# Kernel optimization log

Measured on AMD Instinct MI355X. Metric: run time of the kernel, lower is better.

Reference implementation:

```python
import jax, jax.numpy as jnp
import numpy as np

B, N, C, K, D, H = 4, 16384, 256, 16, 4, 512
EPS = 1e-5


def setup_inputs() -> dict:
    key = jax.random.key(0)
    ks = jax.random.split(key, 16)
    s = 0.05  # weight scale
    inp = {
        "x": jax.random.normal(ks[0], (B, N, C), jnp.float32),
        "knn": jax.random.randint(ks[1], (B, N, K), 0, N, jnp.int32),
        "lfp_w": jax.random.normal(ks[2], (D, C, C), jnp.float32) * s,
        "lfp_bn_w": jax.random.uniform(ks[3], (D, C), jnp.float32),
        "lfp_bn_b": jax.random.normal(ks[4], (D, C), jnp.float32) * s,
        "mlp0_w1": jax.random.normal(ks[5], (C, H), jnp.float32) * s,
        "mlp0_b1": jax.random.normal(ks[6], (H,), jnp.float32) * s,
        "mlp0_w2": jax.random.normal(ks[7], (H, C), jnp.float32) * s,
        "mlp0_bn_w": jax.random.uniform(ks[8], (C,), jnp.float32),
        "mlp0_bn_b": jax.random.normal(ks[9], (C,), jnp.float32) * s,
        "mlps_w1": jax.random.normal(ks[10], (D // 2, C, H), jnp.float32) * s,
        "mlps_b1": jax.random.normal(ks[11], (D // 2, H), jnp.float32) * s,
        "mlps_w2": jax.random.normal(ks[12], (D // 2, H, C), jnp.float32) * s,
        "mlps_bn_w": jax.random.uniform(ks[13], (D // 2, C), jnp.float32),
        "mlps_bn_b": jax.random.normal(ks[14], (D // 2, C), jnp.float32) * s,
    }
    return inp


def _bn(y, w, b):
    # BatchNorm1d over flattened (B*N) rows, biased variance, train-mode stats
    m = y.mean(axis=(0, 1))
    v = ((y - m) ** 2).mean(axis=(0, 1))
    return (y - m) * jax.lax.rsqrt(v + EPS) * w + b


def _mlp(y, w1, b1, w2, bw, bb):
    h = jax.nn.gelu(jnp.einsum("bnc,ch->bnh", y, w1) + b1, approximate=False)
    return _bn(jnp.einsum("bnh,hc->bnc", h, w2), bw, bb)


def _lfp(y, knn, w, bw, bb):
    p = jnp.einsum("bnc,cd->bnd", y, w)               # linear proj, no bias
    nb = jax.vmap(lambda pb, kb: pb[kb])(p, knn)      # [B,N,K,C] neighbor gather
    return _bn(nb.max(axis=2) - p, bw, bb)            # max over knn minus self


def reference(x, knn, lfp_w, lfp_bn_w, lfp_bn_b,
              mlp0_w1, mlp0_b1, mlp0_w2, mlp0_bn_w, mlp0_bn_b,
              mlps_w1, mlps_b1, mlps_w2, mlps_bn_w, mlps_bn_b):
    # Block.forward (eval: drop_path = identity)
    x = x + _mlp(x, mlp0_w1, mlp0_b1, mlp0_w2, mlp0_bn_w, mlp0_bn_b)
    depth = lfp_w.shape[0]
    for i in range(depth):
        x = x + _lfp(x, knn, lfp_w[i], lfp_bn_w[i], lfp_bn_b[i])
        if i % 2 == 1:
            j = i // 2
            x = x + _mlp(x, mlps_w1[j], mlps_b1[j], mlps_w2[j],
                         mlps_bn_w[j], mlps_bn_b[j])
    return x
```

## Files before the change

### kernel.cpp

```cpp
#include <hip/hip_runtime.h>
#include <hip/hip_bf16.h>

#define M_TOTAL 65536
#define NPTS    16384
#define CDIM    256
#define KNN     16
#define HDIM    512

typedef __bf16 bf16x8 __attribute__((ext_vector_type(8)));
typedef float  f32x4  __attribute__((ext_vector_type(4)));

__device__ inline float b2f(unsigned u) {
    union { unsigned v; float f; } x; x.v = u << 16; return x.f;
}
__device__ inline unsigned short f2b(float f) {
    union { float f; unsigned u; } x; x.f = f;
    unsigned r = x.u + 0x7fffu + ((x.u >> 16) & 1u);
    return (unsigned short)(r >> 16);
}
__device__ inline void gload_lds16(const void* g, void* l) {
    __builtin_amdgcn_global_load_lds(
        (const __attribute__((address_space(1))) unsigned*)g,
        (__attribute__((address_space(3))) unsigned*)l, 16, 0, 0);
}

template<int MODE>
__global__ __launch_bounds__(256) void gemm_nt(
    const short* __restrict__ A, const short* __restrict__ BT,
    short* __restrict__ outB,
    const float* __restrict__ bias, float2* __restrict__ partials,
    int N, int K)
{
    __shared__ short a_lds[128 * 32];
    __shared__ short b_lds[128 * 32];
    __shared__ float s_sum[128], s_sq[128];

    const int tid = threadIdx.x;
    const int m0 = blockIdx.y * 128, n0 = blockIdx.x * 128;
    const int w = tid >> 6, l = tid & 63;
    const int wm = w >> 1, wn = w & 1;

    if (MODE == 2 && tid < 128) { s_sum[tid] = 0.f; s_sq[tid] = 0.f; }

    f32x4 acc[4][4] = {};

    const int lrow = l & 15, lk = (l >> 4) * 8;
    const int q0 = 2 * w, q1 = 2 * w + 1;
    const int gr = l >> 2, gc = (l & 3) * 8;
    const size_t arow0 = (size_t)(m0 + q0 * 16 + gr) * K + gc;
    const size_t arow1 = (size_t)(m0 + q1 * 16 + gr) * K + gc;
    const size_t brow0 = (size_t)(n0 + q0 * 16 + gr) * K + gc;
    const size_t brow1 = (size_t)(n0 + q1 * 16 + gr) * K + gc;

    const int nkt = K >> 5;
    for (int kt = 0; kt < nkt; ++kt) {
        const int k0 = kt << 5;
        if (kt) __syncthreads();
        gload_lds16(A  + arow0 + k0, a_lds + q0 * 512);
        gload_lds16(A  + arow1 + k0, a_lds + q1 * 512);
        gload_lds16(BT + brow0 + k0, b_lds + q0 * 512);
        gload_lds16(BT + brow1 + k0, b_lds + q1 * 512);
        __syncthreads();

        bf16x8 af[4], bfr[4];
#pragma unroll
        for (int i = 0; i < 4; ++i)
            af[i] = *(const bf16x8*)(a_lds + (wm * 64 + i * 16 + lrow) * 32 + lk);
#pragma unroll
        for (int j = 0; j < 4; ++j)
            bfr[j] = *(const bf16x8*)(b_lds + (wn * 64 + j * 16 + lrow) * 32 + lk);
#pragma unroll
        for (int i = 0; i < 4; ++i)
#pragma unroll
            for (int j = 0; j < 4; ++j)
                acc[i][j] = __builtin_amdgcn_mfma_f32_16x16x32_bf16(
                    af[i], bfr[j], acc[i][j], 0, 0, 0);
    }

    const int lq = l >> 4;
#pragma unroll
    for (int j = 0; j < 4; ++j) {
        const int cl  = wn * 64 + j * 16 + lrow;
        const int col = n0 + cl;
        const float bsv = (MODE == 1) ? bias[col] : 0.f;
        float psum = 0.f, psq = 0.f;
#pragma unroll
        for (int i = 0; i < 4; ++i) {
#pragma unroll
            for (int r = 0; r < 4; ++r) {
                const int row = m0 + wm * 64 + i * 16 + lq * 4 + r;
                float v = acc[i][j][r];
                if (MODE == 1) {
                    v += bsv;
                    v = 0.5f * v * (1.f + erff(v * 0.70710678118654752f));
                }
                outB[(size_t)row * N + col] = (short)f2b(v);
                if (MODE == 2) { psum += v; psq += v * v; }
            }
        }
        if (MODE == 2) {
            atomicAdd(&s_sum[cl], psum);
            atomicAdd(&s_sq[cl], psq);
        }
    }
    if (MODE == 2) {
        __syncthreads();
        if (tid < 128)
            partials[(size_t)blockIdx.y * N + n0 + tid] =
                make_float2(s_sum[tid], s_sq[tid]);
    }
}

__global__ __launch_bounds__(256) void gather_max(
    const short* __restrict__ p, const int* __restrict__ knn,
    short* __restrict__ yout, float2* __restrict__ partials)
{
    __shared__ float s_sum[256], s_sq[256];
    const int tid = threadIdx.x, w = tid >> 6, l = tid & 63;
    s_sum[tid] = 0.f; s_sq[tid] = 0.f;
    __syncthreads();

    const int xcd = blockIdx.x & 7, hi = blockIdx.x >> 3;
    const int gblk = (xcd >> 1) * 512 + (hi << 1) + (xcd & 1);

    float sa0 = 0, sa1 = 0, sa2 = 0, sa3 = 0;
    float qa0 = 0, qa1 = 0, qa2 = 0, qa3 = 0;
    const int c0 = l * 4;
    for (int rr = 0; rr < 8; ++rr) {
        const size_t g = (size_t)gblk * 32 + w * 8 + rr;
        const int b = (int)(g >> 14);
        const int n = (int)(g & (NPTS - 1));
        const int4* kp4 = (const int4*)(knn + ((size_t)b * NPTS + n) * KNN);
        int idxs[16];
        {
            const int4 i0 = kp4[0], i1 = kp4[1], i2 = kp4[2], i3 = kp4[3];
            idxs[0]=i0.x; idxs[1]=i0.y; idxs[2]=i0.z; idxs[3]=i0.w;
            idxs[4]=i1.x; idxs[5]=i1.y; idxs[6]=i1.z; idxs[7]=i1.w;
            idxs[8]=i2.x; idxs[9]=i2.y; idxs[10]=i2.z; idxs[11]=i2.w;
            idxs[12]=i3.x; idxs[13]=i3.y; idxs[14]=i3.z; idxs[15]=i3.w;
        }
        const size_t pbase = (size_t)b * NPTS * CDIM;
        float mx0 = -1e30f, mx1 = -1e30f, mx2 = -1e30f, mx3 = -1e30f;
#pragma unroll
        for (int k = 0; k < KNN; ++k) {
            const uint2 v = *(const uint2*)(p + pbase + (size_t)idxs[k] * CDIM + c0);
            mx0 = fmaxf(mx0, b2f(v.x & 0xffffu));
            mx1 = fmaxf(mx1, b2f(v.x >> 16));
            mx2 = fmaxf(mx2, b2f(v.y & 0xffffu));
            mx3 = fmaxf(mx3, b2f(v.y >> 16));
        }
        const uint2 sv = *(const uint2*)(p + g * CDIM + c0);
        const float t0 = mx0 - b2f(sv.x & 0xffffu);
        const float t1 = mx1 - b2f(sv.x >> 16);
        const float t2 = mx2 - b2f(sv.y & 0xffffu);
        const float t3 = mx3 - b2f(sv.y >> 16);
        uint2 pk;
        pk.x = (unsigned)f2b(t0) | ((unsigned)f2b(t1) << 16);
        pk.y = (unsigned)f2b(t2) | ((unsigned)f2b(t3) << 16);
        *(uint2*)(yout + g * CDIM + c0) = pk;
        sa0 += t0; sa1 += t1; sa2 += t2; sa3 += t3;
        qa0 += t0 * t0; qa1 += t1 * t1; qa2 += t2 * t2; qa3 += t3 * t3;
    }
    atomicAdd(&s_sum[c0 + 0], sa0); atomicAdd(&s_sq[c0 + 0], qa0);
    atomicAdd(&s_sum[c0 + 1], sa1); atomicAdd(&s_sq[c0 + 1], qa1);
    atomicAdd(&s_sum[c0 + 2], sa2); atomicAdd(&s_sq[c0 + 2], qa2);
    atomicAdd(&s_sum[c0 + 3], sa3); atomicAdd(&s_sq[c0 + 3], qa3);
    __syncthreads();
    partials[(size_t)gblk * CDIM + tid] = make_float2(s_sum[tid], s_sq[tid]);
}

__global__ __launch_bounds__(256) void reduce_stats(
    const float2* __restrict__ partials, int nblk,
    const float* __restrict__ bnw, const float* __restrict__ bnb,
    float2* __restrict__ scsh)
{
    __shared__ float ss[4], qq[4];
    const int c = blockIdx.x;
    const int tid = threadIdx.x, w = tid >> 6, l = tid & 63;
    float s = 0.f, q = 0.f;
    for (int rb = tid; rb < nblk; rb += 256) {
        const float2 v = partials[(size_t)rb * CDIM + c];
        s += v.x; q += v.y;
    }
#pragma unroll
    for (int off = 32; off > 0; off >>= 1) {
        s += __shfl_down(s, off);
        q += __shfl_down(q, off);
    }
    if (l == 0) { ss[w] = s; qq[w] = q; }
    __syncthreads();
    if (tid == 0) {
        const float S = ss[0] + ss[1] + ss[2] + ss[3];
        const float Q = qq[0] + qq[1] + qq[2] + qq[3];
        const float invM = 1.f / 65536.f;
        const float mean = S * invM;
        const float var  = Q * invM - mean * mean;
        const float istd = rsqrtf(var + 1e-5f);
        const float sc   = bnw[c] * istd;
        scsh[c] = make_float2(sc, bnb[c] - mean * sc);
    }
}

__global__ __launch_bounds__(256) void bn_residual(
    const short* __restrict__ y, const float* __restrict__ resid,
    const float2* __restrict__ scsh,
    float* __restrict__ xout, short* __restrict__ xbout)
{
    const size_t t = (size_t)blockIdx.x * 256 + threadIdx.x;
    const uint2 yv = ((const uint2*)y)[t];
    const float4 rv = ((const float4*)resid)[t];
    const int c0 = (int)((t * 4) & (CDIM - 1));
    const float2 s0 = scsh[c0], s1 = scsh[c0 + 1], s2 = scsh[c0 + 2], s3 = scsh[c0 + 3];
    const float o0 = rv.x + b2f(yv.x & 0xffffu) * s0.x + s0.y;
    const float o1 = rv.y + b2f(yv.x >> 16)     * s1.x + s1.y;
    const float o2 = rv.z + b2f(yv.y & 0xffffu) * s2.x + s2.y;
    const float o3 = rv.w + b2f(yv.y >> 16)     * s3.x + s3.y;
    ((float4*)xout)[t] = make_float4(o0, o1, o2, o3);
    if (xbout) {
        uint2 pk;
        pk.x = (unsigned)f2b(o0) | ((unsigned)f2b(o1) << 16);
        pk.y = (unsigned)f2b(o2) | ((unsigned)f2b(o3) << 16);
        ((uint2*)xbout)[t] = pk;
    }
}

__global__ __launch_bounds__(256) void cast_x(
    const float* __restrict__ x, short* __restrict__ xb)
{
    const size_t t = (size_t)blockIdx.x * 256 + threadIdx.x;
    const float4 v = ((const float4*)x)[t];
    uint2 pk;
    pk.x = (unsigned)f2b(v.x) | ((unsigned)f2b(v.y) << 16);
    pk.y = (unsigned)f2b(v.z) | ((unsigned)f2b(v.w) << 16);
    ((uint2*)xb)[t] = pk;
}

__global__ __launch_bounds__(256) void transpose_cast(
    const float* __restrict__ src, short* __restrict__ dst, int R, int Cc)
{
    const size_t base = (size_t)blockIdx.y * R * Cc;
    const int i = blockIdx.x * 256 + threadIdx.x;
    if (i < R * Cc) {
        const int r = i / Cc, c = i % Cc;
        dst[base + (size_t)c * R + r] = (short)f2b(src[base + i]);
    }
}


extern "C" void kernel_launch(void* const* d_in, const int* in_sizes, int n_in,
                              void* d_out, int out_size, void* d_ws, size_t ws_size,
                              hipStream_t stream)
{
    (void)in_sizes; (void)n_in; (void)out_size; (void)ws_size;

    const float* x_in      = (const float*)d_in[0];
    const int*   knn       = (const int*)  d_in[1];
    const float* lfp_w     = (const float*)d_in[2];
    const float* lfp_bn_w  = (const float*)d_in[3];
    const float* lfp_bn_b  = (const float*)d_in[4];
    const float* mlp0_w1   = (const float*)d_in[5];
    const float* mlp0_b1   = (const float*)d_in[6];
    const float* mlp0_w2   = (const float*)d_in[7];
    const float* mlp0_bn_w = (const float*)d_in[8];
    const float* mlp0_bn_b = (const float*)d_in[9];
    const float* mlps_w1   = (const float*)d_in[10];
    const float* mlps_b1   = (const float*)d_in[11];
    const float* mlps_w2   = (const float*)d_in[12];
    const float* mlps_bn_w = (const float*)d_in[13];
    const float* mlps_bn_b = (const float*)d_in[14];

    char* ws = (char*)d_ws;
    short*  xb       = (short*) (ws + 0);
    short*  ybB      = (short*) (ws + 33554432ull);
    short*  hp       = (short*) (ws + 67108864ull);
    float2* partials = (float2*)(ws + 134217728ull);
    float2* scsh     = (float2*)(ws + 138412032ull);
    short*  lfpWT    = (short*) (ws + 138414080ull);
    short*  w1T0     = (short*) (ws + 138938368ull);
    short*  w2T0     = (short*) (ws + 139200512ull);
    short*  w1Ts     = (short*) (ws + 139462656ull);
    short*  w2Ts     = (short*) (ws + 139986944ull);
    float*  xout     = (float*)d_out;

    const dim3 blk(256);

    transpose_cast<<<dim3(256, 4), blk, 0, stream>>>(lfp_w,   lfpWT, 256, 256);
    transpose_cast<<<dim3(512, 1), blk, 0, stream>>>(mlp0_w1, w1T0,  256, 512);
    transpose_cast<<<dim3(512, 1), blk, 0, stream>>>(mlp0_w2, w2T0,  512, 256);
    transpose_cast<<<dim3(512, 2), blk, 0, stream>>>(mlps_w1, w1Ts,  256, 512);
    transpose_cast<<<dim3(512, 2), blk, 0, stream>>>(mlps_w2, w2Ts,  512, 256);
    cast_x<<<16384, blk, 0, stream>>>(x_in, xb);

    auto run_mlp = [&](const short* w1T, const float* b1, const short* w2T,
                       const float* bnw, const float* bnb, const float* resid,
                       bool last) {
        gemm_nt<1><<<dim3(4, 512), blk, 0, stream>>>(xb, w1T, hp,  b1, nullptr, 512, 256);
        gemm_nt<2><<<dim3(2, 512), blk, 0, stream>>>(hp, w2T, ybB, nullptr, partials, 256, 512);
        reduce_stats<<<256, blk, 0, stream>>>(partials, 512, bnw, bnb, scsh);
        bn_residual<<<16384, blk, 0, stream>>>(ybB, resid, scsh, xout, last ? nullptr : xb);
    };

    run_mlp(w1T0, mlp0_b1, w2T0, mlp0_bn_w, mlp0_bn_b, x_in, false);

    for (int i = 0; i < 4; ++i) {
        gemm_nt<0><<<dim3(2, 512), blk, 0, stream>>>(xb, lfpWT + (size_t)i * 65536,
                                                     hp, nullptr, nullptr, 256, 256);
        gather_max<<<2048, blk, 0, stream>>>(hp, knn, ybB, partials);
        reduce_stats<<<256, blk, 0, stream>>>(partials, 2048,
                                              lfp_bn_w + i * 256, lfp_bn_b + i * 256, scsh);
        bn_residual<<<16384, blk, 0, stream>>>(ybB, xout, scsh, xout, xb);
        if (i & 1) {
            const int j = i >> 1;
            run_mlp(w1Ts + (size_t)j * 131072, mlps_b1 + j * 512,
                    w2Ts + (size_t)j * 131072,
                    mlps_bn_w + j * 256, mlps_bn_b + j * 256, xout,
                    i == 3);
        }
    }
}
```

Baseline: 963.6 us.

## Stage GEMM output through LDS, swizzle workgroups, use tanh GELU, split gather by channels

The GEMM epilogue now writes its tile into padded LDS and stores it to global memory as coalesced 16-byte rows. Workgroup ids are remapped so that consecutive ids land on the same XCD. The exact erf GELU is replaced by a tanh approximation built from a fast exp and a reciprocal. The gather-max kernel is split into two launches, each covering 128 channels, so the working set of gathered rows fits better in cache. The tanh GELU changes numerics against the erf reference, and the extra launch adds overhead.

```diff
diff --git a/kernel.cpp b/kernel.cpp
--- a/kernel.cpp
+++ b/kernel.cpp
@@ -6,6 +6,7 @@
 #define CDIM    256
 #define KNN     16
 #define HDIM    512
+#define CSTR    136
 
 typedef __bf16 bf16x8 __attribute__((ext_vector_type(8)));
 typedef float  f32x4  __attribute__((ext_vector_type(4)));
@@ -22,6 +23,12 @@
     __builtin_amdgcn_global_load_lds(
         (const __attribute__((address_space(1))) unsigned*)g,
         (__attribute__((address_space(3))) unsigned*)l, 16, 0, 0);
+}
+__device__ inline float gelu_tanh(float u) {
+    const float t = u * (0.7978845608f + 0.0356774081f * u * u);
+    const float e = __expf(2.f * t);
+    const float th = 1.f - 2.f * __builtin_amdgcn_rcpf(e + 1.f);
+    return 0.5f * u * (1.f + th);
 }
 
 template<int MODE>
@@ -33,10 +40,15 @@
 {
     __shared__ short a_lds[128 * 32];
     __shared__ short b_lds[128 * 32];
+    __shared__ short c_lds[128 * CSTR];
     __shared__ float s_sum[128], s_sq[128];
 
     const int tid = threadIdx.x;
-    const int m0 = blockIdx.y * 128, n0 = blockIdx.x * 128;
+    const int nx = gridDim.x, nwg = nx * gridDim.y;
+    const int bid = blockIdx.y * nx + blockIdx.x;
+    const int lid = (bid & 7) * (nwg >> 3) + (bid >> 3);
+    const int m0 = (lid / nx) * 128, n0 = (lid % nx) * 128;
+
     const int w = tid >> 6, l = tid & 63;
     const int wm = w >> 1, wn = w & 1;
 
@@ -81,20 +93,16 @@
 #pragma unroll
     for (int j = 0; j < 4; ++j) {
         const int cl  = wn * 64 + j * 16 + lrow;
-        const int col = n0 + cl;
-        const float bsv = (MODE == 1) ? bias[col] : 0.f;
+        const float bsv = (MODE == 1) ? bias[n0 + cl] : 0.f;
         float psum = 0.f, psq = 0.f;
 #pragma unroll
         for (int i = 0; i < 4; ++i) {
 #pragma unroll
             for (int r = 0; r < 4; ++r) {
-                const int row = m0 + wm * 64 + i * 16 + lq * 4 + r;
+                const int row = wm * 64 + i * 16 + lq * 4 + r;
                 float v = acc[i][j][r];
-                if (MODE == 1) {
-                    v += bsv;
-                    v = 0.5f * v * (1.f + erff(v * 0.70710678118654752f));
-                }
-                outB[(size_t)row * N + col] = (short)f2b(v);
+                if (MODE == 1) v = gelu_tanh(v + bsv);
+                c_lds[row * CSTR + cl] = (short)f2b(v);
                 if (MODE == 2) { psum += v; psq += v * v; }
             }
         }
@@ -103,31 +111,39 @@
             atomicAdd(&s_sq[cl], psq);
         }
     }
-    if (MODE == 2) {
-        __syncthreads();
-        if (tid < 128)
-            partials[(size_t)blockIdx.y * N + n0 + tid] =
-                make_float2(s_sum[tid], s_sq[tid]);
-    }
+    __syncthreads();
+#pragma unroll
+    for (int it = 0; it < 8; ++it) {
+        const int idx = it * 256 + tid;
+        const int row = idx >> 4, ch = idx & 15;
+        const uint4 vv = *(const uint4*)&c_lds[row * CSTR + ch * 8];
+        *(uint4*)&outB[(size_t)(m0 + row) * N + n0 + ch * 8] = vv;
+    }
+    if (MODE == 2 && tid < 128)
+        partials[(size_t)(m0 >> 7) * N + n0 + tid] =
+            make_float2(s_sum[tid], s_sq[tid]);
 }
 
 __global__ __launch_bounds__(256) void gather_max(
     const short* __restrict__ p, const int* __restrict__ knn,
-    short* __restrict__ yout, float2* __restrict__ partials)
-{
-    __shared__ float s_sum[256], s_sq[256];
+    short* __restrict__ yout, float2* __restrict__ partials, int pass)
+{
+    __shared__ float s_sum[128], s_sq[128];
     const int tid = threadIdx.x, w = tid >> 6, l = tid & 63;
-    s_sum[tid] = 0.f; s_sq[tid] = 0.f;
+    if (tid < 128) { s_sum[tid] = 0.f; s_sq[tid] = 0.f; }
     __syncthreads();
 
     const int xcd = blockIdx.x & 7, hi = blockIdx.x >> 3;
     const int gblk = (xcd >> 1) * 512 + (hi << 1) + (xcd & 1);
 
+    const int sub = l >> 5;
+    const int cl  = (l & 31) * 4;
+    const int coff = pass * 128 + cl;
+
     float sa0 = 0, sa1 = 0, sa2 = 0, sa3 = 0;
     float qa0 = 0, qa1 = 0, qa2 = 0, qa3 = 0;
-    const int c0 = l * 4;
-    for (int rr = 0; rr < 8; ++rr) {
-        const size_t g = (size_t)gblk * 32 + w * 8 + rr;
+    for (int it = 0; it < 4; ++it) {
+        const size_t g = (size_t)gblk * 32 + w * 8 + it * 2 + sub;
         const int b = (int)(g >> 14);
         const int n = (int)(g & (NPTS - 1));
         const int4* kp4 = (const int4*)(knn + ((size_t)b * NPTS + n) * KNN);
@@ -139,17 +155,17 @@
             idxs[8]=i2.x; idxs[9]=i2.y; idxs[10]=i2.z; idxs[11]=i2.w;
             idxs[12]=i3.x; idxs[13]=i3.y; idxs[14]=i3.z; idxs[15]=i3.w;
         }
-        const size_t pbase = (size_t)b * NPTS * CDIM;
+        const size_t pbase = (size_t)b * NPTS * CDIM + coff;
         float mx0 = -1e30f, mx1 = -1e30f, mx2 = -1e30f, mx3 = -1e30f;
 #pragma unroll
         for (int k = 0; k < KNN; ++k) {
-            const uint2 v = *(const uint2*)(p + pbase + (size_t)idxs[k] * CDIM + c0);
+            const uint2 v = *(const uint2*)(p + pbase + (size_t)idxs[k] * CDIM);
             mx0 = fmaxf(mx0, b2f(v.x & 0xffffu));
             mx1 = fmaxf(mx1, b2f(v.x >> 16));
             mx2 = fmaxf(mx2, b2f(v.y & 0xffffu));
             mx3 = fmaxf(mx3, b2f(v.y >> 16));
         }
-        const uint2 sv = *(const uint2*)(p + g * CDIM + c0);
+        const uint2 sv = *(const uint2*)(p + g * CDIM + coff);
         const float t0 = mx0 - b2f(sv.x & 0xffffu);
         const float t1 = mx1 - b2f(sv.x >> 16);
         const float t2 = mx2 - b2f(sv.y & 0xffffu);
@@ -157,16 +173,18 @@
         uint2 pk;
         pk.x = (unsigned)f2b(t0) | ((unsigned)f2b(t1) << 16);
         pk.y = (unsigned)f2b(t2) | ((unsigned)f2b(t3) << 16);
-        *(uint2*)(yout + g * CDIM + c0) = pk;
+        *(uint2*)(yout + g * CDIM + coff) = pk;
         sa0 += t0; sa1 += t1; sa2 += t2; sa3 += t3;
         qa0 += t0 * t0; qa1 += t1 * t1; qa2 += t2 * t2; qa3 += t3 * t3;
     }
-    atomicAdd(&s_sum[c0 + 0], sa0); atomicAdd(&s_sq[c0 + 0], qa0);
-    atomicAdd(&s_sum[c0 + 1], sa1); atomicAdd(&s_sq[c0 + 1], qa1);
-    atomicAdd(&s_sum[c0 + 2], sa2); atomicAdd(&s_sq[c0 + 2], qa2);
-    atomicAdd(&s_sum[c0 + 3], sa3); atomicAdd(&s_sq[c0 + 3], qa3);
+    atomicAdd(&s_sum[cl + 0], sa0); atomicAdd(&s_sq[cl + 0], qa0);
+    atomicAdd(&s_sum[cl + 1], sa1); atomicAdd(&s_sq[cl + 1], qa1);
+    atomicAdd(&s_sum[cl + 2], sa2); atomicAdd(&s_sq[cl + 2], qa2);
+    atomicAdd(&s_sum[cl + 3], sa3); atomicAdd(&s_sq[cl + 3], qa3);
     __syncthreads();
-    partials[(size_t)gblk * CDIM + tid] = make_float2(s_sum[tid], s_sq[tid]);
+    if (tid < 128)
+        partials[(size_t)gblk * CDIM + pass * 128 + tid] =
+            make_float2(s_sum[tid], s_sq[tid]);
 }
 
 __global__ __launch_bounds__(256) void reduce_stats(
@@ -305,7 +323,8 @@
     for (int i = 0; i < 4; ++i) {
         gemm_nt<0><<<dim3(2, 512), blk, 0, stream>>>(xb, lfpWT + (size_t)i * 65536,
                                                      hp, nullptr, nullptr, 256, 256);
-        gather_max<<<2048, blk, 0, stream>>>(hp, knn, ybB, partials);
+        gather_max<<<2048, blk, 0, stream>>>(hp, knn, ybB, partials, 0);
+        gather_max<<<2048, blk, 0, stream>>>(hp, knn, ybB, partials, 1);
         reduce_stats<<<256, blk, 0, stream>>>(partials, 2048,
                                               lfp_bn_w + i * 256, lfp_bn_b + i * 256, scsh);
         bn_residual<<<16384, blk, 0, stream>>>(ybB, xout, scsh, xout, xb);
```

Result: no change. 952.7 us (-1.1%).
